# Optimization experiments

Hardware: AMD Instinct MI355X
Metric: run time of the kernel (lower is better)

## Reference

```python
import jax, jax.numpy as jnp
import numpy as np

D, P, N = 256, 32, 262144


def setup_inputs() -> dict:
    key = jax.random.key(0)
    k1, k2, k3 = jax.random.split(key, 3)
    ZPi = jax.random.normal(k1, (D + P, N), dtype=jnp.float32)
    U = jax.random.normal(k2, (D, P), dtype=jnp.float32) / np.float32(np.sqrt(D))
    alpha = jax.random.normal(k3, (P,), dtype=jnp.float32)
    return {"ZPi": ZPi, "U": U, "alpha": alpha}


def reference(ZPi, U, alpha):
    # CCLayer forward. U: (D,p), alpha: (p,), ZPi: (D+p, N).
    d, p = U.shape
    Z = ZPi[:d, :]        # (D, N)
    Pi = ZPi[d:, :]       # (p, N)
    if p == 1:
        return Z - U @ (U.T @ Z)
    # Original builds (D,N,p) intermediates:
    #   affine_proj[d,n,k] = Z[d,n] - U[d,k]*(U^T Z)[k,n] + (U*alpha)[d,k]
    #   Z_out[d,n] = sum_k affine_proj[d,n,k] * Pi[k,n]
    # Algebraically equivalent GEMM form (same math, no 3D intermediate):
    UtZ = U.T @ Z                      # (p, N)
    sum_pi = Pi.sum(axis=0)            # (N,)
    Z_out = Z * sum_pi[None, :] - U @ (UtZ * Pi) + (U * alpha[None, :]) @ Pi
    return jnp.vstack((Z_out, Pi))
```

## Files before the change

kernel.cpp:

```cpp
#include <hip/hip_runtime.h>
#include <stdint.h>


#define NCOLS 262144
#define DROWS 256
#define PROWS 32
#define TILE  128
#define NWAVE 4
#define RPW   64

typedef float v2f __attribute__((ext_vector_type(2)));

__global__ __launch_bounds__(256, 4) void CCLayer_kernel(
    const float* __restrict__ ZPi,
    const float* __restrict__ U,
    const float* __restrict__ alpha,
    float* __restrict__ out)
{
    __shared__ float wbuf[PROWS][TILE];
    __shared__ float sp[NWAVE][TILE];

    const int lane = threadIdx.x & 63;
    const int q    = __builtin_amdgcn_readfirstlane((int)(threadIdx.x >> 6));
    const int n0   = blockIdx.x * TILE;
    const int c0   = lane * 2;
    const size_t gc = (size_t)n0 + c0;

    {
        float4* wb4 = (float4*)&wbuf[0][0];
        #pragma unroll
        for (int i = 0; i < 4; ++i)
            wb4[threadIdx.x + 256 * i] = make_float4(0.f, 0.f, 0.f, 0.f);
    }

    v2f pi[8];
    v2f ps = {0.f, 0.f};
    #pragma unroll
    for (int j = 0; j < 8; ++j) {
        const int p = q * 8 + j;
        const size_t off = (size_t)(DROWS + p) * NCOLS + gc;
        const v2f v = *(const v2f*)(ZPi + off);
        pi[j] = v;
        __builtin_nontemporal_store(v, (v2f*)(out + off));
        ps += v;
    }
    sp[q][c0]     = ps.x;
    sp[q][c0 + 1] = ps.y;

    __syncthreads();

    v2f utz[PROWS];
    #pragma unroll
    for (int p = 0; p < PROWS; ++p) utz[p] = (v2f){0.f, 0.f};

    const float* zbase = ZPi + (size_t)(q * RPW) * NCOLS + gc;
    const float* ubase = U + q * RPW * PROWS;

    #pragma unroll 8
    for (int d = 0; d < RPW; ++d) {
        const v2f z2 = *(const v2f*)(zbase + (size_t)d * NCOLS);
        const float* urow = ubase + d * PROWS;
        #pragma unroll
        for (int p = 0; p < PROWS; ++p) {
            utz[p].x = __builtin_fmaf(urow[p], z2.x, utz[p].x);
            utz[p].y = __builtin_fmaf(urow[p], z2.y, utz[p].y);
        }
    }
    #pragma unroll
    for (int p = 0; p < PROWS; ++p) {
        atomicAdd(&wbuf[p][c0],     utz[p].x);
        atomicAdd(&wbuf[p][c0 + 1], utz[p].y);
    }

    __syncthreads();

    #pragma unroll
    for (int j = 0; j < 8; ++j) {
        const int p = q * 8 + j;
        const float a = alpha[p];
        wbuf[p][c0]     = (a - wbuf[p][c0])     * pi[j].x;
        wbuf[p][c0 + 1] = (a - wbuf[p][c0 + 1]) * pi[j].y;
    }

    __syncthreads();

    v2f s2 = {0.f, 0.f};
    #pragma unroll
    for (int qq = 0; qq < NWAVE; ++qq) {
        s2.x += sp[qq][c0];
        s2.y += sp[qq][c0 + 1];
    }
    v2f w[PROWS];
    #pragma unroll
    for (int p = 0; p < PROWS; ++p)
        w[p] = *(const v2f*)&wbuf[p][c0];

    float* obase = out + (size_t)(q * RPW) * NCOLS + gc;
    #pragma unroll 8
    for (int d = 0; d < RPW; ++d) {
        const v2f z2 = *(const v2f*)(zbase + (size_t)d * NCOLS);
        const float* urow = ubase + d * PROWS;
        v2f acc = {s2.x * z2.x, s2.y * z2.y};
        #pragma unroll
        for (int p = 0; p < PROWS; ++p) {
            acc.x = __builtin_fmaf(urow[p], w[p].x, acc.x);
            acc.y = __builtin_fmaf(urow[p], w[p].y, acc.y);
        }
        __builtin_nontemporal_store(acc, (v2f*)(obase + (size_t)d * NCOLS));
    }
}

extern "C" void kernel_launch(void* const* d_in, const int* in_sizes, int n_in,
                              void* d_out, int out_size, void* d_ws, size_t ws_size,
                              hipStream_t stream) {
    const float* ZPi   = (const float*)d_in[0];
    const float* U     = (const float*)d_in[1];
    const float* alpha = (const float*)d_in[2];
    float* out = (float*)d_out;

    dim3 grid(NCOLS / TILE);
    dim3 block(256);
    CCLayer_kernel<<<grid, block, 0, stream>>>(ZPi, U, alpha, out);
}
```

Before: 665.3 us.

## Double-buffer Z row loads in registers and stage Pi through shared memory

Adds register double-buffering of Z rows in chunks of eight, so the next chunk's global loads are issued before the FMAs on the current chunk, in both the U^T Z pass and the output pass. The first chunk is loaded before the Pi copy, and reloaded ahead of the barrier for the second pass, to overlap memory latency with other work. Pi values are now kept in a new shared buffer rather than registers and are read with nontemporal loads. This frees the Pi registers, but the double buffers raise register pressure under launch_bounds(256,4) and shared memory use grows.

```diff
diff --git a/kernel.cpp b/kernel.cpp
--- a/kernel.cpp
+++ b/kernel.cpp
@@ -8,6 +8,8 @@
 #define TILE  128
 #define NWAVE 4
 #define RPW   64
+#define CHUNK 8
+#define NCHUNK (RPW / CHUNK)
 
 typedef float v2f __attribute__((ext_vector_type(2)));
 
@@ -18,6 +20,7 @@
     float* __restrict__ out)
 {
     __shared__ float wbuf[PROWS][TILE];
+    __shared__ float pibuf[PROWS][TILE];
     __shared__ float sp[NWAVE][TILE];
 
     const int lane = threadIdx.x & 63;
@@ -26,6 +29,29 @@
     const int c0   = lane * 2;
     const size_t gc = (size_t)n0 + c0;
 
+    const float* zbase = ZPi + (size_t)(q * RPW) * NCOLS + gc;
+    const float* ubase = U + q * RPW * PROWS;
+
+    v2f zb0[CHUNK], zb1[CHUNK];
+    #pragma unroll
+    for (int i = 0; i < CHUNK; ++i)
+        zb0[i] = *(const v2f*)(zbase + (size_t)i * NCOLS);
+
+    {
+        v2f ps = {0.f, 0.f};
+        #pragma unroll
+        for (int j = 0; j < 8; ++j) {
+            const int p = q * 8 + j;
+            const size_t off = (size_t)(DROWS + p) * NCOLS + gc;
+            const v2f v = __builtin_nontemporal_load((const v2f*)(ZPi + off));
+            __builtin_nontemporal_store(v, (v2f*)(out + off));
+            *(v2f*)&pibuf[p][c0] = v;
+            ps += v;
+        }
+        sp[q][c0]     = ps.x;
+        sp[q][c0 + 1] = ps.y;
+    }
+
     {
         float4* wb4 = (float4*)&wbuf[0][0];
         #pragma unroll
@@ -33,37 +59,31 @@
             wb4[threadIdx.x + 256 * i] = make_float4(0.f, 0.f, 0.f, 0.f);
     }
 
-    v2f pi[8];
-    v2f ps = {0.f, 0.f};
-    #pragma unroll
-    for (int j = 0; j < 8; ++j) {
-        const int p = q * 8 + j;
-        const size_t off = (size_t)(DROWS + p) * NCOLS + gc;
-        const v2f v = *(const v2f*)(ZPi + off);
-        pi[j] = v;
-        __builtin_nontemporal_store(v, (v2f*)(out + off));
-        ps += v;
-    }
-    sp[q][c0]     = ps.x;
-    sp[q][c0 + 1] = ps.y;
-
     __syncthreads();
 
     v2f utz[PROWS];
     #pragma unroll
     for (int p = 0; p < PROWS; ++p) utz[p] = (v2f){0.f, 0.f};
 
-    const float* zbase = ZPi + (size_t)(q * RPW) * NCOLS + gc;
-    const float* ubase = U + q * RPW * PROWS;
-
-    #pragma unroll 8
-    for (int d = 0; d < RPW; ++d) {
-        const v2f z2 = *(const v2f*)(zbase + (size_t)d * NCOLS);
-        const float* urow = ubase + d * PROWS;
+    #pragma unroll
+    for (int c = 0; c < NCHUNK; ++c) {
+        v2f* cur = (c & 1) ? zb1 : zb0;
+        v2f* nxt = (c & 1) ? zb0 : zb1;
+        if (c + 1 < NCHUNK) {
+            #pragma unroll
+            for (int i = 0; i < CHUNK; ++i)
+                nxt[i] = *(const v2f*)(zbase + (size_t)((c + 1) * CHUNK + i) * NCOLS);
+        }
         #pragma unroll
-        for (int p = 0; p < PROWS; ++p) {
-            utz[p].x = __builtin_fmaf(urow[p], z2.x, utz[p].x);
-            utz[p].y = __builtin_fmaf(urow[p], z2.y, utz[p].y);
+        for (int i = 0; i < CHUNK; ++i) {
+            const int d = c * CHUNK + i;
+            const float* urow = ubase + d * PROWS;
+            const v2f z2 = cur[i];
+            #pragma unroll
+            for (int p = 0; p < PROWS; ++p) {
+                utz[p].x = __builtin_fmaf(urow[p], z2.x, utz[p].x);
+                utz[p].y = __builtin_fmaf(urow[p], z2.y, utz[p].y);
+            }
         }
     }
     #pragma unroll
@@ -72,14 +92,18 @@
         atomicAdd(&wbuf[p][c0 + 1], utz[p].y);
     }
 
+    #pragma unroll
+    for (int i = 0; i < CHUNK; ++i)
+        zb0[i] = *(const v2f*)(zbase + (size_t)i * NCOLS);
+
     __syncthreads();
 
     #pragma unroll
     for (int j = 0; j < 8; ++j) {
         const int p = q * 8 + j;
         const float a = alpha[p];
-        wbuf[p][c0]     = (a - wbuf[p][c0])     * pi[j].x;
-        wbuf[p][c0 + 1] = (a - wbuf[p][c0 + 1]) * pi[j].y;
+        wbuf[p][c0]     = (a - wbuf[p][c0])     * pibuf[p][c0];
+        wbuf[p][c0 + 1] = (a - wbuf[p][c0 + 1]) * pibuf[p][c0 + 1];
     }
 
     __syncthreads();
@@ -96,17 +120,28 @@
         w[p] = *(const v2f*)&wbuf[p][c0];
 
     float* obase = out + (size_t)(q * RPW) * NCOLS + gc;
-    #pragma unroll 8
-    for (int d = 0; d < RPW; ++d) {
-        const v2f z2 = *(const v2f*)(zbase + (size_t)d * NCOLS);
-        const float* urow = ubase + d * PROWS;
-        v2f acc = {s2.x * z2.x, s2.y * z2.y};
+    #pragma unroll
+    for (int c = 0; c < NCHUNK; ++c) {
+        v2f* cur = (c & 1) ? zb1 : zb0;
+        v2f* nxt = (c & 1) ? zb0 : zb1;
+        if (c + 1 < NCHUNK) {
+            #pragma unroll
+            for (int i = 0; i < CHUNK; ++i)
+                nxt[i] = *(const v2f*)(zbase + (size_t)((c + 1) * CHUNK + i) * NCOLS);
+        }
         #pragma unroll
-        for (int p = 0; p < PROWS; ++p) {
-            acc.x = __builtin_fmaf(urow[p], w[p].x, acc.x);
-            acc.y = __builtin_fmaf(urow[p], w[p].y, acc.y);
+        for (int i = 0; i < CHUNK; ++i) {
+            const int d = c * CHUNK + i;
+            const float* urow = ubase + d * PROWS;
+            const v2f z2 = cur[i];
+            v2f acc = {s2.x * z2.x, s2.y * z2.y};
+            #pragma unroll
+            for (int p = 0; p < PROWS; ++p) {
+                acc.x = __builtin_fmaf(urow[p], w[p].x, acc.x);
+                acc.y = __builtin_fmaf(urow[p], w[p].y, acc.y);
+            }
+            __builtin_nontemporal_store(acc, (v2f*)(obase + (size_t)d * NCOLS));
         }
-        __builtin_nontemporal_store(acc, (v2f*)(obase + (size_t)d * NCOLS));
     }
 }
 
```

Result: slower. 936.3 us (+40.7%).
